# Optimization experiments

Hardware: AMD Instinct MI355X
Metric: run time of the kernel (lower is better)

## Reference

```python
import jax, jax.numpy as jnp
import numpy as np

N_NODES = 100000
N_EDGES = 1600000
IN_DIM = 64
HID = 128
OUT_DIM = 2
N_GRAPHS = 64


def setup_inputs() -> dict:
    key = jax.random.key(0)
    ks = jax.random.split(key, 9)
    x = jax.random.normal(ks[0], (N_NODES, IN_DIM), dtype=jnp.float32)
    edge_index = jax.random.randint(ks[1], (2, N_EDGES), 0, N_NODES, dtype=jnp.int64)
    batch = jnp.sort(jax.random.randint(ks[2], (N_NODES,), 0, N_GRAPHS, dtype=jnp.int64))
    # GCNConv weights (Glorot-ish scale) and biases
    W1 = jax.random.normal(ks[3], (IN_DIM, HID), dtype=jnp.float32) / np.sqrt(IN_DIM)
    b1 = jnp.zeros((HID,), dtype=jnp.float32)
    W2 = jax.random.normal(ks[4], (HID, HID), dtype=jnp.float32) / np.sqrt(HID)
    b2 = jnp.zeros((HID,), dtype=jnp.float32)
    Wfc = jax.random.normal(ks[5], (HID, OUT_DIM), dtype=jnp.float32) / np.sqrt(HID)
    bfc = jnp.zeros((OUT_DIM,), dtype=jnp.float32)
    return {"x": x, "W1": W1, "b1": b1, "W2": W2, "b2": b2,
            "Wfc": Wfc, "bfc": bfc, "edge_index": edge_index, "batch": batch}


def _gcn_conv(x, W, b, src, dst, num_nodes):
    # PyG GCNConv: linear transform, add self loops, symmetric deg norm, scatter-add.
    h = x @ W  # [N, F]
    loop = jnp.arange(num_nodes, dtype=src.dtype)
    s = jnp.concatenate([src, loop])  # source (message origin)
    d = jnp.concatenate([dst, loop])  # target (aggregation)
    deg = jax.ops.segment_sum(jnp.ones_like(d, dtype=h.dtype), d, num_segments=num_nodes)
    dinv = jnp.where(deg > 0, jax.lax.rsqrt(deg), 0.0)
    norm = dinv[s] * dinv[d]  # [E+N]
    msg = h[s] * norm[:, None]
    out = jax.ops.segment_sum(msg, d, num_segments=num_nodes)
    return out + b


def reference(x, W1, b1, W2, b2, Wfc, bfc, edge_index, batch):
    src, dst = edge_index[0], edge_index[1]
    n = x.shape[0]
    h = jax.nn.relu(_gcn_conv(x, W1, b1, src, dst, n))
    # dropout is a no-op in eval mode
    h = jax.nn.relu(_gcn_conv(h, W2, b2, src, dst, n))
    # global mean pool over graphs
    sums = jax.ops.segment_sum(h, batch, num_segments=N_GRAPHS)
    cnts = jax.ops.segment_sum(jnp.ones((n,), dtype=h.dtype), batch, num_segments=N_GRAPHS)
    pooled = sums / jnp.maximum(cnts, 1.0)[:, None]  # [G, HID]
    logits = pooled @ Wfc + bfc
    return jax.nn.log_softmax(logits, axis=1)
```

## Files before the change

kernel.cpp:

```cpp
#include <hip/hip_runtime.h>
#include <math.h>

#define N_NODES 100000
#define N_EDGES 1600000
#define IN_DIM 64
#define HID 128
#define OUT_DIM 2
#define N_GRAPHS 64

#define NBUK ((N_NODES + 255) / 256)
#define BCAP 4608
#define E4 (N_EDGES / 4)
#define NBLK_P1 ((E4 + 1023) / 1024)

#define PCHUNK 256
#define MAXCH 8

typedef unsigned int uint32;
typedef __attribute__((ext_vector_type(8))) short bf16x8;
typedef __attribute__((ext_vector_type(4))) float f32x4;

static __device__ __forceinline__ ushort f2bf(float f) {
    uint32 u = __float_as_uint(f);
    uint32 r = (u + 0x7fff + ((u >> 16) & 1)) >> 16;
    return (ushort)r;
}
static __device__ __forceinline__ float bf2f(uint32 u) {
    return __uint_as_float(u << 16);
}
static __device__ __forceinline__ float bflo(uint32 u) { return bf2f(u & 0xffffu); }
static __device__ __forceinline__ float bfhi(uint32 u) { return bf2f(u >> 16); }

__global__ __launch_bounds__(1024) void k_pass1(const int4* __restrict__ src4,
                                                const int4* __restrict__ dst4,
                                                int* __restrict__ gcur,
                                                int* __restrict__ bpak) {
    __shared__ int hist[NBUK];
    __shared__ int base[NBUK];
    int tid = threadIdx.x;
    if (tid < NBUK) hist[tid] = 0;
    __syncthreads();
    int i4 = blockIdx.x * 1024 + tid;
    bool act = i4 < E4;
    int4 d = {0, 0, 0, 0}, s = {0, 0, 0, 0};
    if (act) {
        d = dst4[i4];
        s = src4[i4];
        atomicAdd(&hist[d.x >> 8], 1);
        atomicAdd(&hist[d.y >> 8], 1);
        atomicAdd(&hist[d.z >> 8], 1);
        atomicAdd(&hist[d.w >> 8], 1);
    }
    __syncthreads();
    if (tid < NBUK) {
        int c = hist[tid];
        base[tid] = tid * BCAP + (c ? atomicAdd(&gcur[tid], c) : 0);
        hist[tid] = 0;
    }
    __syncthreads();
    if (act) {
        int b0 = d.x >> 8, r0 = atomicAdd(&hist[b0], 1);
        int b1 = d.y >> 8, r1 = atomicAdd(&hist[b1], 1);
        int b2 = d.z >> 8, r2 = atomicAdd(&hist[b2], 1);
        int b3 = d.w >> 8, r3 = atomicAdd(&hist[b3], 1);
        bpak[base[b0] + r0] = ((d.x & 255) << 24) | s.x;
        bpak[base[b1] + r1] = ((d.y & 255) << 24) | s.y;
        bpak[base[b2] + r2] = ((d.z & 255) << 24) | s.z;
        bpak[base[b3] + r3] = ((d.w & 255) << 24) | s.w;
    }
}

__global__ __launch_bounds__(1024) void k_pass2(const int* __restrict__ gcur,
                                                const int* __restrict__ bpak,
                                                const float* __restrict__ x,
                                                int* __restrict__ row_start,
                                                float* __restrict__ dinv,
                                                int* __restrict__ csr,
                                                ushort* __restrict__ xs) {
    __shared__ int cnt[256];
    __shared__ int sc[256];
    __shared__ int lst[256];
    __shared__ float sdinv[256];
    __shared__ int sg[1024];
    __shared__ int sgb;
    int b = blockIdx.x;
    int tid = threadIdx.x;
    int node0 = b * 256;
    int nloc = N_NODES - node0;
    if (nloc > 256) nloc = 256;
    int bbase = b * BCAP;
    int Eb = gcur[b];

    sg[tid] = (tid < NBUK) ? gcur[tid] : 0;
    if (tid < 256) cnt[tid] = 0;
    __syncthreads();
    for (int off = 1; off < 512; off <<= 1) {
        int u = (tid >= off) ? sg[tid - off] : 0;
        __syncthreads();
        sg[tid] += u;
        __syncthreads();
    }
    if (tid == 0) sgb = (b == 0) ? 0 : sg[b - 1];
    __syncthreads();
    int gb = sgb;

    for (int i = tid; i < Eb; i += 1024) atomicAdd(&cnt[(uint32)bpak[bbase + i] >> 24], 1);
    __syncthreads();
    int v = 0;
    if (tid < 256) {
        v = cnt[tid];
        sc[tid] = v;
    }
    __syncthreads();
    for (int off = 1; off < 256; off <<= 1) {
        int u = 0;
        if (tid < 256 && tid >= off) u = sc[tid - off];
        __syncthreads();
        if (tid < 256) sc[tid] += u;
        __syncthreads();
    }
    if (tid < 256) {
        int excl = sc[tid] - v;
        lst[tid] = excl;
        if (tid < nloc) {
            float dv = rsqrtf((float)(v + 1));
            row_start[node0 + tid] = gb + excl;
            dinv[node0 + tid] = dv;
            sdinv[tid] = dv;
        }
        cnt[tid] = 0;
    }
    __syncthreads();
    for (int i = tid; i < Eb; i += 1024) {
        int p = bpak[bbase + i];
        int dl = (uint32)p >> 24;
        int r = atomicAdd(&cnt[dl], 1);
        csr[gb + lst[dl] + r] = p & 0xFFFFFF;
    }
    int f0 = node0 * 16;
    int f1 = (node0 + nloc) * 16;
    for (int idx = f0 + tid; idx < f1; idx += 1024) {
        float dv = sdinv[(idx >> 4) - node0];
        float4 vv = ((const float4*)x)[idx];
        ushort4 o;
        o.x = f2bf(vv.x * dv);
        o.y = f2bf(vv.y * dv);
        o.z = f2bf(vv.z * dv);
        o.w = f2bf(vv.w * dv);
        ((ushort4*)xs)[idx] = o;
    }
}

__global__ __launch_bounds__(256) void k_gbound(const int* __restrict__ batch,
                                                int* __restrict__ gstart,
                                                int* __restrict__ row_start) {
    int n = blockIdx.x * 256 + threadIdx.x;
    if (n >= N_NODES) return;
    if (n == 0) {
        for (int g = 0; g <= batch[0]; ++g) gstart[g] = 0;
    } else {
        int a = batch[n - 1], b = batch[n];
        for (int g = a + 1; g <= b; ++g) gstart[g] = n;
    }
    if (n == N_NODES - 1) {
        for (int g = batch[n] + 1; g <= N_GRAPHS; ++g) gstart[g] = N_NODES;
        row_start[N_NODES] = N_EDGES;
    }
}

__global__ __launch_bounds__(256) void k_agg1(const int* __restrict__ row_start,
                                              const int* __restrict__ csr,
                                              const uint32* __restrict__ xs,
                                              const float* __restrict__ dinv,
                                              uint32* __restrict__ outb) {
    int d = blockIdx.x * 8 + (threadIdx.x >> 5);
    int l = threadIdx.x & 31;
    float dd = dinv[d];
    uint32 u = xs[(long long)d * 32 + l];
    float a0 = bflo(u), a1 = bfhi(u);
    int e = row_start[d];
    int eend = row_start[d + 1];
    for (; e + 7 < eend; e += 8) {
        int s0 = csr[e], s1 = csr[e + 1], s2 = csr[e + 2], s3 = csr[e + 3];
        int s4 = csr[e + 4], s5 = csr[e + 5], s6 = csr[e + 6], s7 = csr[e + 7];
        uint32 w0 = xs[(long long)s0 * 32 + l];
        uint32 w1 = xs[(long long)s1 * 32 + l];
        uint32 w2 = xs[(long long)s2 * 32 + l];
        uint32 w3 = xs[(long long)s3 * 32 + l];
        uint32 w4 = xs[(long long)s4 * 32 + l];
        uint32 w5 = xs[(long long)s5 * 32 + l];
        uint32 w6 = xs[(long long)s6 * 32 + l];
        uint32 w7 = xs[(long long)s7 * 32 + l];
        a0 += ((bflo(w0) + bflo(w1)) + (bflo(w2) + bflo(w3))) +
              ((bflo(w4) + bflo(w5)) + (bflo(w6) + bflo(w7)));
        a1 += ((bfhi(w0) + bfhi(w1)) + (bfhi(w2) + bfhi(w3))) +
              ((bfhi(w4) + bfhi(w5)) + (bfhi(w6) + bfhi(w7)));
    }
    for (; e + 3 < eend; e += 4) {
        int s0 = csr[e], s1 = csr[e + 1], s2 = csr[e + 2], s3 = csr[e + 3];
        uint32 w0 = xs[(long long)s0 * 32 + l];
        uint32 w1 = xs[(long long)s1 * 32 + l];
        uint32 w2 = xs[(long long)s2 * 32 + l];
        uint32 w3 = xs[(long long)s3 * 32 + l];
        a0 += (bflo(w0) + bflo(w1)) + (bflo(w2) + bflo(w3));
        a1 += (bfhi(w0) + bfhi(w1)) + (bfhi(w2) + bfhi(w3));
    }
    for (; e < eend; ++e) {
        uint32 w = xs[(long long)csr[e] * 32 + l];
        a0 += bflo(w);
        a1 += bfhi(w);
    }
    outb[(long long)d * 32 + l] = (uint32)f2bf(a0 * dd) | ((uint32)f2bf(a1 * dd) << 16);
}

__global__ __launch_bounds__(256) void k_agg2(const int* __restrict__ row_start,
                                              const int* __restrict__ csr,
                                              const uint2* __restrict__ hs,
                                              const float* __restrict__ dinv,
                                              uint2* __restrict__ outb) {
    int d = blockIdx.x * 8 + (threadIdx.x >> 5);
    int l = threadIdx.x & 31;
    float dd = dinv[d];
    uint2 u = hs[(long long)d * 32 + l];
    float a0 = bflo(u.x), a1 = bfhi(u.x), a2 = bflo(u.y), a3 = bfhi(u.y);
    int e = row_start[d];
    int eend = row_start[d + 1];
    for (; e + 7 < eend; e += 8) {
        int s0 = csr[e], s1 = csr[e + 1], s2 = csr[e + 2], s3 = csr[e + 3];
        int s4 = csr[e + 4], s5 = csr[e + 5], s6 = csr[e + 6], s7 = csr[e + 7];
        uint2 w0 = hs[(long long)s0 * 32 + l];
        uint2 w1 = hs[(long long)s1 * 32 + l];
        uint2 w2 = hs[(long long)s2 * 32 + l];
        uint2 w3 = hs[(long long)s3 * 32 + l];
        uint2 w4 = hs[(long long)s4 * 32 + l];
        uint2 w5 = hs[(long long)s5 * 32 + l];
        uint2 w6 = hs[(long long)s6 * 32 + l];
        uint2 w7 = hs[(long long)s7 * 32 + l];
        a0 += ((bflo(w0.x) + bflo(w1.x)) + (bflo(w2.x) + bflo(w3.x))) +
              ((bflo(w4.x) + bflo(w5.x)) + (bflo(w6.x) + bflo(w7.x)));
        a1 += ((bfhi(w0.x) + bfhi(w1.x)) + (bfhi(w2.x) + bfhi(w3.x))) +
              ((bfhi(w4.x) + bfhi(w5.x)) + (bfhi(w6.x) + bfhi(w7.x)));
        a2 += ((bflo(w0.y) + bflo(w1.y)) + (bflo(w2.y) + bflo(w3.y))) +
              ((bflo(w4.y) + bflo(w5.y)) + (bflo(w6.y) + bflo(w7.y)));
        a3 += ((bfhi(w0.y) + bfhi(w1.y)) + (bfhi(w2.y) + bfhi(w3.y))) +
              ((bfhi(w4.y) + bfhi(w5.y)) + (bfhi(w6.y) + bfhi(w7.y)));
    }
    for (; e + 3 < eend; e += 4) {
        int s0 = csr[e], s1 = csr[e + 1], s2 = csr[e + 2], s3 = csr[e + 3];
        uint2 w0 = hs[(long long)s0 * 32 + l];
        uint2 w1 = hs[(long long)s1 * 32 + l];
        uint2 w2 = hs[(long long)s2 * 32 + l];
        uint2 w3 = hs[(long long)s3 * 32 + l];
        a0 += (bflo(w0.x) + bflo(w1.x)) + (bflo(w2.x) + bflo(w3.x));
        a1 += (bfhi(w0.x) + bfhi(w1.x)) + (bfhi(w2.x) + bfhi(w3.x));
        a2 += (bflo(w0.y) + bflo(w1.y)) + (bflo(w2.y) + bflo(w3.y));
        a3 += (bfhi(w0.y) + bfhi(w1.y)) + (bfhi(w2.y) + bfhi(w3.y));
    }
    for (; e < eend; ++e) {
        uint2 w = hs[(long long)csr[e] * 32 + l];
        a0 += bflo(w.x);
        a1 += bfhi(w.x);
        a2 += bflo(w.y);
        a3 += bfhi(w.y);
    }
    uint2 o;
    o.x = (uint32)f2bf(a0 * dd) | ((uint32)f2bf(a1 * dd) << 16);
    o.y = (uint32)f2bf(a2 * dd) | ((uint32)f2bf(a3 * dd) << 16);
    outb[(long long)d * 32 + l] = o;
}

template <int K, int OUTM>
__global__ __launch_bounds__(256) void k_gemm_mfma(const ushort* __restrict__ A,
                                                   const float* __restrict__ W,
                                                   const float* __restrict__ bias,
                                                   const float* __restrict__ dinv,
                                                   ushort* __restrict__ outb) {
    constexpr int KSTEPS = K / 32;
    constexpr int LDSK = K + 8;
    __shared__ ushort WT[128 * LDSK];
    int tid = threadIdx.x;
    for (int idx = tid; idx < K * 128; idx += 256) {
        int k = idx >> 7, c = idx & 127;
        WT[c * LDSK + k] = f2bf(W[idx]);
    }
    __syncthreads();

    int w = tid >> 6, l = tid & 63;
    int row0 = blockIdx.x * 64 + w * 16;
    int arow = row0 + (l & 15);
    if (arow > N_NODES - 1) arow = N_NODES - 1;
    int koff = (l >> 4) * 8;

    bf16x8 af[KSTEPS];
#pragma unroll
    for (int ks = 0; ks < KSTEPS; ++ks)
        af[ks] = *(const bf16x8*)(A + (long long)arow * K + ks * 32 + koff);

    f32x4 acc[8];
#pragma unroll
    for (int t = 0; t < 8; ++t) acc[t] = (f32x4){0.f, 0.f, 0.f, 0.f};

#pragma unroll
    for (int ks = 0; ks < KSTEPS; ++ks) {
#pragma unroll
        for (int t = 0; t < 8; ++t) {
            int c = t * 16 + (l & 15);
            bf16x8 bf = *(const bf16x8*)&WT[c * LDSK + ks * 32 + koff];
            acc[t] = __builtin_amdgcn_mfma_f32_16x16x32_bf16(af[ks], bf, acc[t], 0, 0, 0);
        }
    }

    int rbase = row0 + ((l >> 4) << 2);
#pragma unroll
    for (int t = 0; t < 8; ++t) {
        int col = t * 16 + (l & 15);
        float bb = bias[col];
#pragma unroll
        for (int i = 0; i < 4; ++i) {
            int row = rbase + i;
            if (row < N_NODES) {
                float v = acc[t][i] + bb;
                v = v > 0.f ? v : 0.f;
                if (OUTM == 1) v *= dinv[row];
                outb[(long long)row * HID + col] = f2bf(v);
            }
        }
    }
}

__global__ __launch_bounds__(256) void k_pool(const uint32* __restrict__ h2,
                                              const int* __restrict__ gstart,
                                              float* __restrict__ pooled) {
    int g = blockIdx.x >> 3;
    int c = blockIdx.x & (MAXCH - 1);
    int r0 = gstart[g] + c * PCHUNK;
    int r1 = gstart[g + 1];
    if (r0 >= r1) return;
    int rend = r0 + PCHUNK;
    if (rend > r1) rend = r1;
    int j = threadIdx.x & 63;
    int q = threadIdx.x >> 6;
    float a0 = 0.f, a1 = 0.f, b0 = 0.f, b1 = 0.f;
    int r = r0 + q;
    for (; r + 4 < rend; r += 8) {
        uint32 u = h2[(long long)r * 64 + j];
        uint32 v = h2[(long long)(r + 4) * 64 + j];
        a0 += bflo(u);
        a1 += bfhi(u);
        b0 += bflo(v);
        b1 += bfhi(v);
    }
    for (; r < rend; r += 4) {
        uint32 u = h2[(long long)r * 64 + j];
        a0 += bflo(u);
        a1 += bfhi(u);
    }
    __shared__ float red[256][2];
    red[threadIdx.x][0] = a0 + b0;
    red[threadIdx.x][1] = a1 + b1;
    __syncthreads();
    if (q == 0) {
        float s0 = (red[j][0] + red[j + 64][0]) + (red[j + 128][0] + red[j + 192][0]);
        float s1 = (red[j][1] + red[j + 64][1]) + (red[j + 128][1] + red[j + 192][1]);
        atomicAdd(&pooled[g * HID + 2 * j], s0);
        atomicAdd(&pooled[g * HID + 2 * j + 1], s1);
    }
}

__global__ __launch_bounds__(256) void k_head(const float* __restrict__ pooled,
                                              const int* __restrict__ gstart,
                                              const float* __restrict__ Wfc,
                                              const float* __restrict__ bfc,
                                              float* __restrict__ out) {
    int t = threadIdx.x;
    int g = t >> 2, sub = t & 3;
    float inv = 1.0f / fmaxf((float)(gstart[g + 1] - gstart[g]), 1.0f);
    float l0 = 0.f, l1 = 0.f;
    for (int j = sub * 32; j < sub * 32 + 32; ++j) {
        float p = pooled[g * HID + j] * inv;
        l0 += p * Wfc[j * OUT_DIM + 0];
        l1 += p * Wfc[j * OUT_DIM + 1];
    }
    l0 += __shfl_xor(l0, 1);
    l1 += __shfl_xor(l1, 1);
    l0 += __shfl_xor(l0, 2);
    l1 += __shfl_xor(l1, 2);
    if (sub == 0) {
        l0 += bfc[0];
        l1 += bfc[1];
        float m = fmaxf(l0, l1);
        float lse = m + logf(expf(l0 - m) + expf(l1 - m));
        out[g * OUT_DIM + 0] = l0 - lse;
        out[g * OUT_DIM + 1] = l1 - lse;
    }
}

extern "C" void kernel_launch(void* const* d_in, const int* in_sizes, int n_in,
                              void* d_out, int out_size, void* d_ws, size_t ws_size,
                              hipStream_t stream) {
    const float* x   = (const float*)d_in[0];
    const float* W1  = (const float*)d_in[1];
    const float* b1  = (const float*)d_in[2];
    const float* W2  = (const float*)d_in[3];
    const float* b2  = (const float*)d_in[4];
    const float* Wfc = (const float*)d_in[5];
    const float* bfc = (const float*)d_in[6];
    const int* ei    = (const int*)d_in[7];
    const int* batch = (const int*)d_in[8];
    const int* src = ei;
    const int* dst = ei + N_EDGES;
    float* out = (float*)d_out;

    float* bufA = (float*)d_ws;
    float* bufB = bufA + (long long)N_NODES * HID;
    int* bpak = (int*)bufA;
    ushort* agg1o = (ushort*)bufA;
    ushort* agg2o = (ushort*)bufA;
    ushort* xs = (ushort*)bufB;
    ushort* hs = (ushort*)bufB;
    ushort* h2 = (ushort*)bufB;
    int* row_start = (int*)(bufB + (long long)N_NODES * HID);
    float* dinv = (float*)(row_start + N_NODES + 1);
    int* gcur = (int*)(dinv + N_NODES);
    int* gstart = gcur + NBUK;
    int* csr = gstart + (N_GRAPHS + 1);
    float* pooled = (float*)(csr + N_EDGES);

    hipMemsetAsync(gcur, 0, NBUK * sizeof(int), stream);
    hipMemsetAsync(pooled, 0, N_GRAPHS * HID * sizeof(float), stream);
    k_pass1<<<NBLK_P1, 1024, 0, stream>>>((const int4*)src, (const int4*)dst, gcur, bpak);
    k_pass2<<<NBUK, 1024, 0, stream>>>(gcur, bpak, x, row_start, dinv, csr, xs);
    k_gbound<<<(N_NODES + 255) / 256, 256, 0, stream>>>(batch, gstart, row_start);

    const int NGBLK = (N_NODES + 63) / 64;

    k_agg1<<<N_NODES / 8, 256, 0, stream>>>(row_start, csr, (const uint32*)xs, dinv,
                                            (uint32*)agg1o);
    k_gemm_mfma<IN_DIM, 1><<<NGBLK, 256, 0, stream>>>(agg1o, W1, b1, dinv, hs);

    k_agg2<<<N_NODES / 8, 256, 0, stream>>>(row_start, csr, (const uint2*)hs, dinv,
                                            (uint2*)agg2o);
    k_gemm_mfma<HID, 2><<<NGBLK, 256, 0, stream>>>(agg2o, W2, b2, dinv, h2);

    k_pool<<<N_GRAPHS * MAXCH, 256, 0, stream>>>((const uint32*)h2, gstart, pooled);
    k_head<<<1, 256, 0, stream>>>(pooled, gstart, Wfc, bfc, out);
}
```

Measured before the change: 213.9 us.

## Store layer-1 features in column-sliced layout for cache-local layer-2 gather

The first GEMM now writes its bf16 output as eight column slabs of 16 features each, one slab per slice, instead of row-major 128-wide rows. The layer-2 aggregation assigns each block to one slab, with 8 threads per node reading 32 bytes per neighbour. The slab is 3.2 MB, so the random gather working set can fit in cache. The cost is reading the CSR indices eight times, one pass per slab, and a less coalesced strided store in the GEMM epilogue. CSR index loads and the output store are also marked nontemporal.

```diff
diff --git a/kernel.cpp b/kernel.cpp
--- a/kernel.cpp
+++ b/kernel.cpp
@@ -30,6 +30,9 @@
 }
 static __device__ __forceinline__ float bflo(uint32 u) { return bf2f(u & 0xffffu); }
 static __device__ __forceinline__ float bfhi(uint32 u) { return bf2f(u >> 16); }
+static __device__ __forceinline__ uint32 pack2(float a, float b) {
+    return (uint32)f2bf(a) | ((uint32)f2bf(b) << 16);
+}
 
 __global__ __launch_bounds__(1024) void k_pass1(const int4* __restrict__ src4,
                                                 const int4* __restrict__ dst4,
@@ -215,58 +218,49 @@
 
 __global__ __launch_bounds__(256) void k_agg2(const int* __restrict__ row_start,
                                               const int* __restrict__ csr,
-                                              const uint2* __restrict__ hs,
+                                              const uint32* __restrict__ hsl,
                                               const float* __restrict__ dinv,
-                                              uint2* __restrict__ outb) {
-    int d = blockIdx.x * 8 + (threadIdx.x >> 5);
-    int l = threadIdx.x & 31;
+                                              uint32* __restrict__ outb) {
+    int s = blockIdx.x & 7;
+    int nb = blockIdx.x >> 3;
+    int grp = threadIdx.x >> 3;
+    int j = threadIdx.x & 7;
+    int d = nb * 32 + grp;
+    const uint32* tb = hsl + (long long)s * (N_NODES * 8);
     float dd = dinv[d];
-    uint2 u = hs[(long long)d * 32 + l];
-    float a0 = bflo(u.x), a1 = bfhi(u.x), a2 = bflo(u.y), a3 = bfhi(u.y);
+    uint32 u = tb[d * 8 + j];
+    float a0 = bflo(u), a1 = bfhi(u);
     int e = row_start[d];
     int eend = row_start[d + 1];
     for (; e + 7 < eend; e += 8) {
-        int s0 = csr[e], s1 = csr[e + 1], s2 = csr[e + 2], s3 = csr[e + 3];
-        int s4 = csr[e + 4], s5 = csr[e + 5], s6 = csr[e + 6], s7 = csr[e + 7];
-        uint2 w0 = hs[(long long)s0 * 32 + l];
-        uint2 w1 = hs[(long long)s1 * 32 + l];
-        uint2 w2 = hs[(long long)s2 * 32 + l];
-        uint2 w3 = hs[(long long)s3 * 32 + l];
-        uint2 w4 = hs[(long long)s4 * 32 + l];
-        uint2 w5 = hs[(long long)s5 * 32 + l];
-        uint2 w6 = hs[(long long)s6 * 32 + l];
-        uint2 w7 = hs[(long long)s7 * 32 + l];
-        a0 += ((bflo(w0.x) + bflo(w1.x)) + (bflo(w2.x) + bflo(w3.x))) +
-              ((bflo(w4.x) + bflo(w5.x)) + (bflo(w6.x) + bflo(w7.x)));
-        a1 += ((bfhi(w0.x) + bfhi(w1.x)) + (bfhi(w2.x) + bfhi(w3.x))) +
-              ((bfhi(w4.x) + bfhi(w5.x)) + (bfhi(w6.x) + bfhi(w7.x)));
-        a2 += ((bflo(w0.y) + bflo(w1.y)) + (bflo(w2.y) + bflo(w3.y))) +
-              ((bflo(w4.y) + bflo(w5.y)) + (bflo(w6.y) + bflo(w7.y)));
-        a3 += ((bfhi(w0.y) + bfhi(w1.y)) + (bfhi(w2.y) + bfhi(w3.y))) +
-              ((bfhi(w4.y) + bfhi(w5.y)) + (bfhi(w6.y) + bfhi(w7.y)));
-    }
-    for (; e + 3 < eend; e += 4) {
-        int s0 = csr[e], s1 = csr[e + 1], s2 = csr[e + 2], s3 = csr[e + 3];
-        uint2 w0 = hs[(long long)s0 * 32 + l];
-        uint2 w1 = hs[(long long)s1 * 32 + l];
-        uint2 w2 = hs[(long long)s2 * 32 + l];
-        uint2 w3 = hs[(long long)s3 * 32 + l];
-        a0 += (bflo(w0.x) + bflo(w1.x)) + (bflo(w2.x) + bflo(w3.x));
-        a1 += (bfhi(w0.x) + bfhi(w1.x)) + (bfhi(w2.x) + bfhi(w3.x));
-        a2 += (bflo(w0.y) + bflo(w1.y)) + (bflo(w2.y) + bflo(w3.y));
-        a3 += (bfhi(w0.y) + bfhi(w1.y)) + (bfhi(w2.y) + bfhi(w3.y));
+        int s0 = __builtin_nontemporal_load(csr + e);
+        int s1 = __builtin_nontemporal_load(csr + e + 1);
+        int s2 = __builtin_nontemporal_load(csr + e + 2);
+        int s3 = __builtin_nontemporal_load(csr + e + 3);
+        int s4 = __builtin_nontemporal_load(csr + e + 4);
+        int s5 = __builtin_nontemporal_load(csr + e + 5);
+        int s6 = __builtin_nontemporal_load(csr + e + 6);
+        int s7 = __builtin_nontemporal_load(csr + e + 7);
+        uint32 w0 = tb[s0 * 8 + j];
+        uint32 w1 = tb[s1 * 8 + j];
+        uint32 w2 = tb[s2 * 8 + j];
+        uint32 w3 = tb[s3 * 8 + j];
+        uint32 w4 = tb[s4 * 8 + j];
+        uint32 w5 = tb[s5 * 8 + j];
+        uint32 w6 = tb[s6 * 8 + j];
+        uint32 w7 = tb[s7 * 8 + j];
+        a0 += ((bflo(w0) + bflo(w1)) + (bflo(w2) + bflo(w3))) +
+              ((bflo(w4) + bflo(w5)) + (bflo(w6) + bflo(w7)));
+        a1 += ((bfhi(w0) + bfhi(w1)) + (bfhi(w2) + bfhi(w3))) +
+              ((bfhi(w4) + bfhi(w5)) + (bfhi(w6) + bfhi(w7)));
     }
     for (; e < eend; ++e) {
-        uint2 w = hs[(long long)csr[e] * 32 + l];
-        a0 += bflo(w.x);
-        a1 += bfhi(w.x);
-        a2 += bflo(w.y);
-        a3 += bfhi(w.y);
-    }
-    uint2 o;
-    o.x = (uint32)f2bf(a0 * dd) | ((uint32)f2bf(a1 * dd) << 16);
-    o.y = (uint32)f2bf(a2 * dd) | ((uint32)f2bf(a3 * dd) << 16);
-    outb[(long long)d * 32 + l] = o;
+        int s0 = __builtin_nontemporal_load(csr + e);
+        uint32 w = tb[s0 * 8 + j];
+        a0 += bflo(w);
+        a1 += bfhi(w);
+    }
+    __builtin_nontemporal_store(pack2(a0 * dd, a1 * dd), &outb[(long long)d * 64 + s * 8 + j]);
 }
 
 template <int K, int OUTM>
@@ -321,8 +315,12 @@
             if (row < N_NODES) {
                 float v = acc[t][i] + bb;
                 v = v > 0.f ? v : 0.f;
-                if (OUTM == 1) v *= dinv[row];
-                outb[(long long)row * HID + col] = f2bf(v);
+                if (OUTM == 1) {
+                    outb[(long long)t * (N_NODES * 16) + (long long)row * 16 + (l & 15)] =
+                        f2bf(v * dinv[row]);
+                } else {
+                    outb[(long long)row * HID + col] = f2bf(v);
+                }
             }
         }
     }
@@ -438,8 +436,8 @@
                                             (uint32*)agg1o);
     k_gemm_mfma<IN_DIM, 1><<<NGBLK, 256, 0, stream>>>(agg1o, W1, b1, dinv, hs);
 
-    k_agg2<<<N_NODES / 8, 256, 0, stream>>>(row_start, csr, (const uint2*)hs, dinv,
-                                            (uint2*)agg2o);
+    k_agg2<<<(N_NODES / 32) * 8, 256, 0, stream>>>(row_start, csr, (const uint32*)hs, dinv,
+                                                   (uint32*)agg2o);
     k_gemm_mfma<HID, 2><<<NGBLK, 256, 0, stream>>>(agg2o, W2, b2, dinv, h2);
 
     k_pool<<<N_GRAPHS * MAXCH, 256, 0, stream>>>((const uint32*)h2, gstart, pooled);
```

Result: slower. 320.7 us (+50.0%).
